# Performance work log

Measured on AMD Instinct MI355X. Metric: run time of the kernel, lower is better.

## Reference

```python
import jax, jax.numpy as jnp
import numpy as np

HID = 512
VOCAB = 1000


def _lstm_cell(x, h, c, w_ih, w_hh, b_ih, b_hh):
    # torch LSTMCell: gates order i, f, g, o
    gates = x @ w_ih.T + h @ w_hh.T + b_ih + b_hh
    i, f, g, o = jnp.split(gates, 4, axis=-1)
    i = jax.nn.sigmoid(i)
    f = jax.nn.sigmoid(f)
    g = jnp.tanh(g)
    o = jax.nn.sigmoid(o)
    c_new = f * c + i * g
    h_new = o * jnp.tanh(c_new)
    return h_new, c_new


def setup_inputs() -> dict:
    key = jax.random.key(0)
    ks = jax.random.split(key, 16)
    B, R, T = 64, 1024, 200
    s = 0.02
    return {
        "h": jax.random.normal(ks[0], (B, R, HID), dtype=jnp.float32),
        "y": jax.random.randint(ks[1], (B, T), 0, VOCAB, dtype=jnp.int32),
        "phi_w": jax.random.normal(ks[2], (HID, HID), jnp.float32) * s,
        "phi_b": jnp.zeros((HID,), jnp.float32),
        "psi_w": jax.random.normal(ks[3], (HID, HID), jnp.float32) * s,
        "psi_b": jnp.zeros((HID,), jnp.float32),
        "w_ih0": jax.random.normal(ks[4], (4 * HID, HID + VOCAB), jnp.float32) * s,
        "w_hh0": jax.random.normal(ks[5], (4 * HID, HID), jnp.float32) * s,
        "b_ih0": jnp.zeros((4 * HID,), jnp.float32),
        "b_hh0": jnp.zeros((4 * HID,), jnp.float32),
        "w_ih1": jax.random.normal(ks[6], (4 * HID, HID), jnp.float32) * s,
        "w_hh1": jax.random.normal(ks[7], (4 * HID, HID), jnp.float32) * s,
        "b_ih1": jnp.zeros((4 * HID,), jnp.float32),
        "b_hh1": jnp.zeros((4 * HID,), jnp.float32),
        "out_w": jax.random.normal(ks[8], (VOCAB, HID), jnp.float32) * s,
        "out_b": jnp.zeros((VOCAB,), jnp.float32),
    }


def reference(h, y, phi_w, phi_b, psi_w, psi_b,
              w_ih0, w_hh0, b_ih0, b_hh0,
              w_ih1, w_hh1, b_ih1, b_hh1,
              out_w, out_b):
    B = h.shape[0]
    # psi(h) is loop-invariant: precompute once. [B, R, HID]
    hp = h @ psi_w.T + psi_b
    # one-hot targets [T, B, VOCAB] (scan over time axis)
    y_oh = jax.nn.one_hot(y.T, VOCAB, dtype=h.dtype)

    zeros = jnp.zeros((B, HID), h.dtype)

    def step(carry, y_t):
        s0, cs0, s1, cs1 = carry
        # attention context on previous s1
        q = s1 @ phi_w.T + phi_b                  # [B, HID]
        e = jnp.einsum('bd,brd->br', q, hp)       # [B, R]
        alpha = jax.nn.softmax(e, axis=1)
        c = jnp.einsum('br,brd->bd', alpha, hp)   # [B, HID]
        inputs = jnp.concatenate([y_t, c], axis=1)
        s0, cs0 = _lstm_cell(inputs, s0, cs0, w_ih0, w_hh0, b_ih0, b_hh0)
        s1, cs1 = _lstm_cell(s0, s1, cs1, w_ih1, w_hh1, b_ih1, b_hh1)
        return (s0, cs0, s1, cs1), s1

    _, s_seq = jax.lax.scan(step, (zeros, zeros, zeros, zeros), y_oh)
    s_seq = jnp.transpose(s_seq, (1, 0, 2))       # [B, T, HID]
    return s_seq @ out_w.T + out_b                # [B, T, VOCAB]
```

## Files before the change

### kernel.cpp

```cpp
#include <hip/hip_runtime.h>
#include <math.h>

#define BB 64
#define RR 1024
#define TT 200
#define HH 512
#define VV 1000
#define GG 2048

__device__ __forceinline__ float sigmf(float x) { return 1.f / (1.f + __expf(-x)); }

__global__ __launch_bounds__(256) void transpose_k(const float* __restrict__ src,
    float* __restrict__ dst, int Msrc, int Mdst, int N, int sstride, int soff) {
  __shared__ float tile[32][33];
  int mt = blockIdx.y * 32, ntb = blockIdx.x * 32;
  int tx = threadIdx.x & 31, ty = threadIdx.x >> 5;
  #pragma unroll
  for (int i = ty; i < 32; i += 8) {
    int m = mt + i, n = ntb + tx;
    tile[i][tx] = (m < Msrc && n < N) ? src[(size_t)m * sstride + soff + n] : 0.f;
  }
  __syncthreads();
  #pragma unroll
  for (int i = ty; i < 32; i += 8) {
    int n = ntb + i, m = mt + tx;
    if (n < N && m < Mdst) dst[(size_t)n * Mdst + m] = tile[tx][i];
  }
}

__global__ __launch_bounds__(256) void biggemm_k(const float* __restrict__ A,
    const float* __restrict__ W, int wld, const float* __restrict__ bias,
    float* __restrict__ C, int cld, int Nout) {
  int mt = blockIdx.x * 128, nt = blockIdx.y * 64;
  __shared__ float As[16][132];
  __shared__ float Ws[16][68];
  int tid = threadIdx.x;
  int ty = tid >> 4, tx = tid & 15;
  float acc[8][4] = {};
  for (int k0 = 0; k0 < 512; k0 += 16) {
    {
      int kc = (tid & 3) * 4;
      int r0 = tid >> 2;
      #pragma unroll
      for (int hh = 0; hh < 2; hh++) {
        int row = r0 + hh * 64;
        float4 a4 = *(const float4*)&A[(size_t)(mt + row) * 512 + k0 + kc];
        As[kc + 0][row] = a4.x; As[kc + 1][row] = a4.y;
        As[kc + 2][row] = a4.z; As[kc + 3][row] = a4.w;
      }
      int krow = tid >> 4, nc = (tid & 15) * 4;
      *(float4*)&Ws[krow][nc] = *(const float4*)&W[(size_t)(k0 + krow) * wld + nt + nc];
    }
    __syncthreads();
    #pragma unroll
    for (int kk = 0; kk < 16; kk++) {
      float4 a0 = *(float4*)&As[kk][ty * 8];
      float4 a1 = *(float4*)&As[kk][ty * 8 + 4];
      float4 w4 = *(float4*)&Ws[kk][tx * 4];
      float av[8] = {a0.x, a0.y, a0.z, a0.w, a1.x, a1.y, a1.z, a1.w};
      float wv[4] = {w4.x, w4.y, w4.z, w4.w};
      #pragma unroll
      for (int i = 0; i < 8; i++)
        #pragma unroll
        for (int j = 0; j < 4; j++)
          acc[i][j] += av[i] * wv[j];
    }
    __syncthreads();
  }
  #pragma unroll
  for (int i = 0; i < 8; i++) {
    int m = mt + ty * 8 + i;
    #pragma unroll
    for (int j = 0; j < 4; j++) {
      int n = nt + tx * 4 + j;
      if (n < Nout) C[(size_t)m * cld + n] = acc[i][j] + bias[n];
    }
  }
}

__global__ __launch_bounds__(256) void smallgemm_k(
    const float* __restrict__ A1, const float* __restrict__ W1, int wld1,
    const float* __restrict__ A2, const float* __restrict__ W2, int wld2,
    int dual, float* __restrict__ Cpart, int N) {
  int nt = blockIdx.x, kc = blockIdx.y;
  const float *A, *W; int wld, k0;
  if (dual && kc >= 4) { A = A2; W = W2; wld = wld2; k0 = (kc - 4) * 128; }
  else                 { A = A1; W = W1; wld = wld1; k0 = kc * 128; }
  __shared__ float Ask[64][68];
  __shared__ float Ws[64][68];
  int tid = threadIdx.x;
  int bq = tid >> 4, nq = tid & 15;
  int b0 = bq * 4, n0 = nq * 4;
  float acc[4][4] = {};
  for (int kb = 0; kb < 128; kb += 64) {
    {
      int brow = tid & 63;
      int kcb = (tid >> 6) * 16;
      const float* ap = A + (size_t)brow * 512 + k0 + kb + kcb;
      #pragma unroll
      for (int j = 0; j < 4; j++) {
        float4 a4 = *(const float4*)(ap + j * 4);
        Ask[kcb + j * 4 + 0][brow] = a4.x;
        Ask[kcb + j * 4 + 1][brow] = a4.y;
        Ask[kcb + j * 4 + 2][brow] = a4.z;
        Ask[kcb + j * 4 + 3][brow] = a4.w;
      }
      int nc = (tid & 15) * 4;
      #pragma unroll
      for (int j = 0; j < 4; j++) {
        int krow = (tid >> 4) + j * 16;
        *(float4*)&Ws[krow][nc] =
            *(const float4*)&W[(size_t)(k0 + kb + krow) * wld + nt * 64 + nc];
      }
    }
    __syncthreads();
    #pragma unroll
    for (int kk = 0; kk < 64; kk++) {
      float4 a = *(float4*)&Ask[kk][b0];
      float4 w = *(float4*)&Ws[kk][n0];
      acc[0][0] += a.x * w.x; acc[0][1] += a.x * w.y; acc[0][2] += a.x * w.z; acc[0][3] += a.x * w.w;
      acc[1][0] += a.y * w.x; acc[1][1] += a.y * w.y; acc[1][2] += a.y * w.z; acc[1][3] += a.y * w.w;
      acc[2][0] += a.z * w.x; acc[2][1] += a.z * w.y; acc[2][2] += a.z * w.z; acc[2][3] += a.z * w.w;
      acc[3][0] += a.w * w.x; acc[3][1] += a.w * w.y; acc[3][2] += a.w * w.z; acc[3][3] += a.w * w.w;
    }
    __syncthreads();
  }
  float* Cout = Cpart + (size_t)kc * BB * N + (size_t)nt * 64;
  #pragma unroll
  for (int i = 0; i < 4; i++) {
    float4 v = make_float4(acc[i][0], acc[i][1], acc[i][2], acc[i][3]);
    *(float4*)&Cout[(size_t)(b0 + i) * N + n0] = v;
  }
}

__global__ __launch_bounds__(256) void attn_k(const float* __restrict__ hp,
    const float* __restrict__ qpart, const float* __restrict__ phi_b,
    float* __restrict__ partm, float* __restrict__ partl, float* __restrict__ partacc) {
  int b = blockIdx.x >> 3, ch = blockIdx.x & 7;
  __shared__ float qs[HH];
  __shared__ float wacc[4][HH];
  __shared__ float wml[8];
  int tid = threadIdx.x;
  for (int d = tid; d < HH; d += 256) {
    float v = phi_b[d];
    #pragma unroll
    for (int p = 0; p < 4; p++) v += qpart[((size_t)p * BB + b) * HH + d];
    qs[d] = v;
  }
  __syncthreads();
  int wave = tid >> 6, lane = tid & 63;
  float qreg[8];
  {
    const float* qp = qs + lane * 8;
    #pragma unroll
    for (int j = 0; j < 8; j++) qreg[j] = qp[j];
  }
  float m = -INFINITY, l = 0.f;
  float acc[8] = {0, 0, 0, 0, 0, 0, 0, 0};
  const float* hpb = hp + ((size_t)b * RR + ch * 128 + wave * 32) * HH + lane * 8;
  float4 v0 = *(const float4*)hpb;
  float4 v1 = *(const float4*)(hpb + 4);
  for (int i = 0; i < 32; i++) {
    float4 n0v, n1v;
    if (i < 31) {
      n0v = *(const float4*)(hpb + (size_t)(i + 1) * HH);
      n1v = *(const float4*)(hpb + (size_t)(i + 1) * HH + 4);
    }
    float rv[8] = {v0.x, v0.y, v0.z, v0.w, v1.x, v1.y, v1.z, v1.w};
    float d0 = 0.f;
    #pragma unroll
    for (int j = 0; j < 8; j++) d0 += qreg[j] * rv[j];
    #pragma unroll
    for (int off = 32; off > 0; off >>= 1) d0 += __shfl_xor(d0, off, 64);
    float mn = fmaxf(m, d0);
    float sc = __expf(m - mn);
    float w = __expf(d0 - mn);
    l = l * sc + w;
    #pragma unroll
    for (int j = 0; j < 8; j++) acc[j] = acc[j] * sc + w * rv[j];
    m = mn;
    v0 = n0v; v1 = n1v;
  }
  #pragma unroll
  for (int j = 0; j < 8; j++) wacc[wave][lane * 8 + j] = acc[j];
  if (lane == 0) { wml[wave] = m; wml[4 + wave] = l; }
  __syncthreads();
  float M = fmaxf(fmaxf(wml[0], wml[1]), fmaxf(wml[2], wml[3]));
  float e0 = __expf(wml[0] - M), e1 = __expf(wml[1] - M);
  float e2 = __expf(wml[2] - M), e3 = __expf(wml[3] - M);
  if (tid == 0) {
    partm[b * 8 + ch] = M;
    partl[b * 8 + ch] = wml[4] * e0 + wml[5] * e1 + wml[6] * e2 + wml[7] * e3;
  }
  for (int d = tid; d < HH; d += 256) {
    partacc[((size_t)b * 8 + ch) * HH + d] =
        wacc[0][d] * e0 + wacc[1][d] * e1 + wacc[2][d] * e2 + wacc[3][d] * e3;
  }
}

__global__ __launch_bounds__(256) void combine_k(const float* __restrict__ partm,
    const float* __restrict__ partl, const float* __restrict__ partacc,
    float* __restrict__ cbuf) {
  int b = blockIdx.x, tid = threadIdx.x;
  float M = -INFINITY;
  #pragma unroll
  for (int p = 0; p < 8; p++) M = fmaxf(M, partm[b * 8 + p]);
  float sc[8]; float L = 0.f;
  #pragma unroll
  for (int p = 0; p < 8; p++) { sc[p] = __expf(partm[b * 8 + p] - M); L += sc[p] * partl[b * 8 + p]; }
  float inv = 1.f / L;
  for (int d = tid; d < HH; d += 256) {
    float v = 0.f;
    #pragma unroll
    for (int p = 0; p < 8; p++) v += sc[p] * partacc[((size_t)b * 8 + p) * HH + d];
    cbuf[b * HH + d] = v * inv;
  }
}

__global__ __launch_bounds__(256) void act0_k(const float* __restrict__ gpart,
    const float* __restrict__ b_ih, const float* __restrict__ b_hh,
    const float* __restrict__ wyT, const int* __restrict__ y, int t,
    float* __restrict__ s0, float* __restrict__ cs0) {
  int idx = blockIdx.x * 256 + threadIdx.x;
  int b = idx >> 9, jj = idx & 511;
  int yv = y[b * TT + t];
  float g[4];
  #pragma unroll
  for (int gi = 0; gi < 4; gi++) {
    int j = gi * 512 + jj;
    float v = b_ih[j] + b_hh[j] + wyT[(size_t)yv * GG + j];
    #pragma unroll
    for (int p = 0; p < 8; p++) v += gpart[((size_t)p * BB + b) * GG + j];
    g[gi] = v;
  }
  float cn = sigmf(g[1]) * cs0[idx] + sigmf(g[0]) * tanhf(g[2]);
  cs0[idx] = cn;
  s0[idx] = sigmf(g[3]) * tanhf(cn);
}

__global__ __launch_bounds__(256) void act1_k(const float* __restrict__ gpart,
    const float* __restrict__ b_ih, const float* __restrict__ b_hh,
    int t, float* __restrict__ s1, float* __restrict__ cs1, float* __restrict__ s_seq) {
  int idx = blockIdx.x * 256 + threadIdx.x;
  int b = idx >> 9, jj = idx & 511;
  float g[4];
  #pragma unroll
  for (int gi = 0; gi < 4; gi++) {
    int j = gi * 512 + jj;
    float v = b_ih[j] + b_hh[j];
    #pragma unroll
    for (int p = 0; p < 8; p++) v += gpart[((size_t)p * BB + b) * GG + j];
    g[gi] = v;
  }
  float cn = sigmf(g[1]) * cs1[idx] + sigmf(g[0]) * tanhf(g[2]);
  cs1[idx] = cn;
  float h = sigmf(g[3]) * tanhf(cn);
  s1[idx] = h;
  s_seq[((size_t)b * TT + t) * HH + jj] = h;
}

extern "C" void kernel_launch(void* const* d_in, const int* in_sizes, int n_in,
                              void* d_out, int out_size, void* d_ws, size_t ws_size,
                              hipStream_t stream) {
  (void)in_sizes; (void)n_in; (void)out_size; (void)ws_size;
  const float* h     = (const float*)d_in[0];
  const int*   y     = (const int*)d_in[1];
  const float* phi_w = (const float*)d_in[2];
  const float* phi_b = (const float*)d_in[3];
  const float* psi_w = (const float*)d_in[4];
  const float* psi_b = (const float*)d_in[5];
  const float* w_ih0 = (const float*)d_in[6];
  const float* w_hh0 = (const float*)d_in[7];
  const float* b_ih0 = (const float*)d_in[8];
  const float* b_hh0 = (const float*)d_in[9];
  const float* w_ih1 = (const float*)d_in[10];
  const float* w_hh1 = (const float*)d_in[11];
  const float* b_ih1 = (const float*)d_in[12];
  const float* b_hh1 = (const float*)d_in[13];
  const float* out_w = (const float*)d_in[14];
  const float* out_b = (const float*)d_in[15];
  float* out = (float*)d_out;

  float* ws = (float*)d_ws;
  size_t off = 0;
  auto alloc = [&](size_t n) { size_t o = off; off += (n + 63) & ~(size_t)63; return o; };
  float* hp     = ws + alloc((size_t)BB * RR * HH);
  float* psi_wT = ws + alloc(HH * HH);
  float* phi_wT = ws + alloc(HH * HH);
  float* wc0T   = ws + alloc(HH * GG);
  float* whh0T  = ws + alloc(HH * GG);
  float* wih1T  = ws + alloc(HH * GG);
  float* whh1T  = ws + alloc(HH * GG);
  float* wyT    = ws + alloc((size_t)VV * GG);
  float* out_wT = ws + alloc((size_t)HH * 1024);
  float* st     = ws + alloc(4 * BB * HH);
  float* s0 = st, *cs0 = st + BB * HH, *s1 = st + 2 * BB * HH, *cs1 = st + 3 * BB * HH;
  float* qpart  = ws + alloc(4 * BB * HH);
  float* cbuf   = ws + alloc(BB * HH);
  float* g0part = ws + alloc((size_t)8 * BB * GG);
  float* g1part = ws + alloc((size_t)8 * BB * GG);
  float* partm  = ws + alloc(BB * 8);
  float* partl  = ws + alloc(BB * 8);
  float* partacc= ws + alloc((size_t)BB * 8 * HH);
  float* s_seq  = ws + alloc((size_t)BB * TT * HH);

  hipMemsetAsync(st, 0, (size_t)4 * BB * HH * sizeof(float), stream);

  dim3 tb(256);
  transpose_k<<<dim3(16, 16), tb, 0, stream>>>(psi_w, psi_wT, 512, 512, 512, 512, 0);
  transpose_k<<<dim3(16, 16), tb, 0, stream>>>(phi_w, phi_wT, 512, 512, 512, 512, 0);
  transpose_k<<<dim3(16, 64), tb, 0, stream>>>(w_ih0, wc0T, 2048, 2048, 512, 1512, 1000);
  transpose_k<<<dim3(16, 64), tb, 0, stream>>>(w_hh0, whh0T, 2048, 2048, 512, 512, 0);
  transpose_k<<<dim3(16, 64), tb, 0, stream>>>(w_ih1, wih1T, 2048, 2048, 512, 512, 0);
  transpose_k<<<dim3(16, 64), tb, 0, stream>>>(w_hh1, whh1T, 2048, 2048, 512, 512, 0);
  transpose_k<<<dim3(32, 64), tb, 0, stream>>>(w_ih0, wyT, 2048, 2048, 1000, 1512, 0);
  transpose_k<<<dim3(16, 32), tb, 0, stream>>>(out_w, out_wT, 1000, 1024, 512, 512, 0);

  biggemm_k<<<dim3(512, 8), tb, 0, stream>>>(h, psi_wT, 512, psi_b, hp, 512, 512);

  for (int t = 0; t < TT; t++) {
    smallgemm_k<<<dim3(8, 4), tb, 0, stream>>>(s1, phi_wT, 512, s1, phi_wT, 512, 0, qpart, 512);
    attn_k<<<dim3(512), tb, 0, stream>>>(hp, qpart, phi_b, partm, partl, partacc);
    combine_k<<<dim3(64), tb, 0, stream>>>(partm, partl, partacc, cbuf);
    smallgemm_k<<<dim3(32, 8), tb, 0, stream>>>(cbuf, wc0T, 2048, s0, whh0T, 2048, 1, g0part, 2048);
    act0_k<<<dim3(128), tb, 0, stream>>>(g0part, b_ih0, b_hh0, wyT, y, t, s0, cs0);
    smallgemm_k<<<dim3(32, 8), tb, 0, stream>>>(s0, wih1T, 2048, s1, whh1T, 2048, 1, g1part, 2048);
    act1_k<<<dim3(128), tb, 0, stream>>>(g1part, b_ih1, b_hh1, t, s1, cs1, s_seq);
  }

  biggemm_k<<<dim3(100, 16), tb, 0, stream>>>(s_seq, out_wT, 1024, out_b, out, 1000, 1000);
}
```

Before: 12.00 ms.

## Hoist recurrent-state GEMMs into one early launch and fuse attention combine into context GEMM

Each timestep's work is reorganized into fewer launches. A single early kernel computes the phi query projection and both hidden-to-hidden gate products (s0@Whh0, s1@Whh1), which depend only on the previous state. The attention softmax combine is fused into the context×Wc0 GEMM, removing the cbuf round trip. The remaining per-step GEMM handles only s0@Wih1. Separately, the big GEMM now uses a 128x128 tile with an 8x8 per-thread micro-tile, which raises register pressure.

After: 13.53 ms. 1.13x slower.

```diff
diff --git a/kernel.cpp b/kernel.cpp
--- a/kernel.cpp
+++ b/kernel.cpp
@@ -31,38 +31,36 @@
 __global__ __launch_bounds__(256) void biggemm_k(const float* __restrict__ A,
     const float* __restrict__ W, int wld, const float* __restrict__ bias,
     float* __restrict__ C, int cld, int Nout) {
-  int mt = blockIdx.x * 128, nt = blockIdx.y * 64;
+  int mt = blockIdx.x * 128, ntile = blockIdx.y * 128;
   __shared__ float As[16][132];
-  __shared__ float Ws[16][68];
+  __shared__ float Ws[16][132];
   int tid = threadIdx.x;
   int ty = tid >> 4, tx = tid & 15;
-  float acc[8][4] = {};
+  float acc[8][8] = {};
   for (int k0 = 0; k0 < 512; k0 += 16) {
     {
-      int kc = (tid & 3) * 4;
-      int r0 = tid >> 2;
-      #pragma unroll
-      for (int hh = 0; hh < 2; hh++) {
-        int row = r0 + hh * 64;
-        float4 a4 = *(const float4*)&A[(size_t)(mt + row) * 512 + k0 + kc];
-        As[kc + 0][row] = a4.x; As[kc + 1][row] = a4.y;
-        As[kc + 2][row] = a4.z; As[kc + 3][row] = a4.w;
-      }
-      int krow = tid >> 4, nc = (tid & 15) * 4;
-      *(float4*)&Ws[krow][nc] = *(const float4*)&W[(size_t)(k0 + krow) * wld + nt + nc];
+      int row = tid >> 1, kc = (tid & 1) * 8;
+      float4 a0 = *(const float4*)&A[(size_t)(mt + row) * 512 + k0 + kc];
+      float4 a1 = *(const float4*)&A[(size_t)(mt + row) * 512 + k0 + kc + 4];
+      As[kc + 0][row] = a0.x; As[kc + 1][row] = a0.y; As[kc + 2][row] = a0.z; As[kc + 3][row] = a0.w;
+      As[kc + 4][row] = a1.x; As[kc + 5][row] = a1.y; As[kc + 6][row] = a1.z; As[kc + 7][row] = a1.w;
+      int krow = tid >> 4, nc = (tid & 15) * 8;
+      *(float4*)&Ws[krow][nc]     = *(const float4*)&W[(size_t)(k0 + krow) * wld + ntile + nc];
+      *(float4*)&Ws[krow][nc + 4] = *(const float4*)&W[(size_t)(k0 + krow) * wld + ntile + nc + 4];
     }
     __syncthreads();
     #pragma unroll
     for (int kk = 0; kk < 16; kk++) {
       float4 a0 = *(float4*)&As[kk][ty * 8];
       float4 a1 = *(float4*)&As[kk][ty * 8 + 4];
-      float4 w4 = *(float4*)&Ws[kk][tx * 4];
+      float4 w0 = *(float4*)&Ws[kk][tx * 8];
+      float4 w1 = *(float4*)&Ws[kk][tx * 8 + 4];
       float av[8] = {a0.x, a0.y, a0.z, a0.w, a1.x, a1.y, a1.z, a1.w};
-      float wv[4] = {w4.x, w4.y, w4.z, w4.w};
+      float wv[8] = {w0.x, w0.y, w0.z, w0.w, w1.x, w1.y, w1.z, w1.w};
       #pragma unroll
       for (int i = 0; i < 8; i++)
         #pragma unroll
-        for (int j = 0; j < 4; j++)
+        for (int j = 0; j < 8; j++)
           acc[i][j] += av[i] * wv[j];
     }
     __syncthreads();
@@ -71,66 +69,96 @@
   for (int i = 0; i < 8; i++) {
     int m = mt + ty * 8 + i;
     #pragma unroll
-    for (int j = 0; j < 4; j++) {
-      int n = nt + tx * 4 + j;
+    for (int j = 0; j < 8; j++) {
+      int n = ntile + tx * 8 + j;
       if (n < Nout) C[(size_t)m * cld + n] = acc[i][j] + bias[n];
     }
   }
 }
 
-__global__ __launch_bounds__(256) void smallgemm_k(
-    const float* __restrict__ A1, const float* __restrict__ W1, int wld1,
-    const float* __restrict__ A2, const float* __restrict__ W2, int wld2,
-    int dual, float* __restrict__ Cpart, int N) {
+#define SG_BODY(Aptr, Wptr, wldv, k0v, Coutp, Nv, ntv)                                        \
+  {                                                                                           \
+    int tid = threadIdx.x;                                                                    \
+    int bq = tid >> 4, nq = tid & 15;                                                         \
+    int b0 = bq * 4, n0 = nq * 4;                                                             \
+    float acc[4][4] = {};                                                                     \
+    for (int kb = 0; kb < 128; kb += 64) {                                                    \
+      {                                                                                       \
+        int brow = tid & 63;                                                                  \
+        int kcb = (tid >> 6) * 16;                                                            \
+        const float* ap = (Aptr) + (size_t)brow * 512 + (k0v) + kb + kcb;                     \
+        _Pragma("unroll")                                                                     \
+        for (int j = 0; j < 4; j++) {                                                         \
+          float4 a4 = *(const float4*)(ap + j * 4);                                           \
+          Ask[kcb + j * 4 + 0][brow] = a4.x;                                                  \
+          Ask[kcb + j * 4 + 1][brow] = a4.y;                                                  \
+          Ask[kcb + j * 4 + 2][brow] = a4.z;                                                  \
+          Ask[kcb + j * 4 + 3][brow] = a4.w;                                                  \
+        }                                                                                     \
+        int nc = (tid & 15) * 4;                                                              \
+        _Pragma("unroll")                                                                     \
+        for (int j = 0; j < 4; j++) {                                                         \
+          int krow = (tid >> 4) + j * 16;                                                     \
+          *(float4*)&Wsk[krow][nc] =                                                          \
+              *(const float4*)&(Wptr)[(size_t)((k0v) + kb + krow) * (wldv) + (ntv)*64 + nc];  \
+        }                                                                                     \
+      }                                                                                       \
+      __syncthreads();                                                                        \
+      _Pragma("unroll")                                                                       \
+      for (int kk = 0; kk < 64; kk++) {                                                       \
+        float4 a = *(float4*)&Ask[kk][b0];                                                    \
+        float4 w = *(float4*)&Wsk[kk][n0];                                                    \
+        acc[0][0] += a.x * w.x; acc[0][1] += a.x * w.y; acc[0][2] += a.x * w.z; acc[0][3] += a.x * w.w; \
+        acc[1][0] += a.y * w.x; acc[1][1] += a.y * w.y; acc[1][2] += a.y * w.z; acc[1][3] += a.y * w.w; \
+        acc[2][0] += a.z * w.x; acc[2][1] += a.z * w.y; acc[2][2] += a.z * w.z; acc[2][3] += a.z * w.w; \
+        acc[3][0] += a.w * w.x; acc[3][1] += a.w * w.y; acc[3][2] += a.w * w.z; acc[3][3] += a.w * w.w; \
+      }                                                                                       \
+      __syncthreads();                                                                        \
+    }                                                                                         \
+    float* Cout2 = (Coutp) + (size_t)(ntv)*64;                                                \
+    _Pragma("unroll")                                                                         \
+    for (int i = 0; i < 4; i++) {                                                             \
+      float4 v = make_float4(acc[i][0], acc[i][1], acc[i][2], acc[i][3]);                     \
+      *(float4*)&Cout2[(size_t)(b0 + i) * (Nv) + n0] = v;                                     \
+    }                                                                                         \
+  }
+
+__global__ __launch_bounds__(256) void earlygemm_k(
+    const float* __restrict__ s0, const float* __restrict__ s1,
+    const float* __restrict__ phi_wT, const float* __restrict__ whh0T,
+    const float* __restrict__ whh1T,
+    float* __restrict__ qpart, float* __restrict__ g0part, float* __restrict__ g1part) {
+  __shared__ float Ask[64][68];
+  __shared__ float Wsk[64][68];
+  int bid = blockIdx.x;
+  const float *A, *W;
+  float* Cout;
+  int wld, k0, N, nt;
+  if (bid < 32) {
+    nt = bid & 7; int kc = bid >> 3;
+    A = s1; W = phi_wT; wld = 512; N = 512; k0 = kc * 128;
+    Cout = qpart + (size_t)kc * BB * 512;
+  } else if (bid < 160) {
+    int idx = bid - 32; nt = idx & 31; int kc = idx >> 5;
+    A = s0; W = whh0T; wld = GG; N = GG; k0 = kc * 128;
+    Cout = g0part + (size_t)(4 + kc) * BB * GG;
+  } else {
+    int idx = bid - 160; nt = idx & 31; int kc = idx >> 5;
+    A = s1; W = whh1T; wld = GG; N = GG; k0 = kc * 128;
+    Cout = g1part + (size_t)(4 + kc) * BB * GG;
+  }
+  SG_BODY(A, W, wld, k0, Cout, N, nt)
+}
+
+__global__ __launch_bounds__(256) void lategemm_k(
+    const float* __restrict__ s0, const float* __restrict__ wih1T,
+    float* __restrict__ g1part) {
+  __shared__ float Ask[64][68];
+  __shared__ float Wsk[64][68];
   int nt = blockIdx.x, kc = blockIdx.y;
-  const float *A, *W; int wld, k0;
-  if (dual && kc >= 4) { A = A2; W = W2; wld = wld2; k0 = (kc - 4) * 128; }
-  else                 { A = A1; W = W1; wld = wld1; k0 = kc * 128; }
-  __shared__ float Ask[64][68];
-  __shared__ float Ws[64][68];
-  int tid = threadIdx.x;
-  int bq = tid >> 4, nq = tid & 15;
-  int b0 = bq * 4, n0 = nq * 4;
-  float acc[4][4] = {};
-  for (int kb = 0; kb < 128; kb += 64) {
-    {
-      int brow = tid & 63;
-      int kcb = (tid >> 6) * 16;
-      const float* ap = A + (size_t)brow * 512 + k0 + kb + kcb;
-      #pragma unroll
-      for (int j = 0; j < 4; j++) {
-        float4 a4 = *(const float4*)(ap + j * 4);
-        Ask[kcb + j * 4 + 0][brow] = a4.x;
-        Ask[kcb + j * 4 + 1][brow] = a4.y;
-        Ask[kcb + j * 4 + 2][brow] = a4.z;
-        Ask[kcb + j * 4 + 3][brow] = a4.w;
-      }
-      int nc = (tid & 15) * 4;
-      #pragma unroll
-      for (int j = 0; j < 4; j++) {
-        int krow = (tid >> 4) + j * 16;
-        *(float4*)&Ws[krow][nc] =
-            *(const float4*)&W[(size_t)(k0 + kb + krow) * wld + nt * 64 + nc];
-      }
-    }
-    __syncthreads();
-    #pragma unroll
-    for (int kk = 0; kk < 64; kk++) {
-      float4 a = *(float4*)&Ask[kk][b0];
-      float4 w = *(float4*)&Ws[kk][n0];
-      acc[0][0] += a.x * w.x; acc[0][1] += a.x * w.y; acc[0][2] += a.x * w.z; acc[0][3] += a.x * w.w;
-      acc[1][0] += a.y * w.x; acc[1][1] += a.y * w.y; acc[1][2] += a.y * w.z; acc[1][3] += a.y * w.w;
-      acc[2][0] += a.z * w.x; acc[2][1] += a.z * w.y; acc[2][2] += a.z * w.z; acc[2][3] += a.z * w.w;
-      acc[3][0] += a.w * w.x; acc[3][1] += a.w * w.y; acc[3][2] += a.w * w.z; acc[3][3] += a.w * w.w;
-    }
-    __syncthreads();
-  }
-  float* Cout = Cpart + (size_t)kc * BB * N + (size_t)nt * 64;
-  #pragma unroll
-  for (int i = 0; i < 4; i++) {
-    float4 v = make_float4(acc[i][0], acc[i][1], acc[i][2], acc[i][3]);
-    *(float4*)&Cout[(size_t)(b0 + i) * N + n0] = v;
-  }
+  int k0 = kc * 128;
+  float* Cout = g1part + (size_t)kc * BB * GG;
+  SG_BODY(s0, wih1T, GG, k0, Cout, GG, nt)
 }
 
 __global__ __launch_bounds__(256) void attn_k(const float* __restrict__ hp,
@@ -198,22 +226,79 @@
   }
 }
 
-__global__ __launch_bounds__(256) void combine_k(const float* __restrict__ partm,
-    const float* __restrict__ partl, const float* __restrict__ partacc,
-    float* __restrict__ cbuf) {
-  int b = blockIdx.x, tid = threadIdx.x;
-  float M = -INFINITY;
-  #pragma unroll
-  for (int p = 0; p < 8; p++) M = fmaxf(M, partm[b * 8 + p]);
-  float sc[8]; float L = 0.f;
-  #pragma unroll
-  for (int p = 0; p < 8; p++) { sc[p] = __expf(partm[b * 8 + p] - M); L += sc[p] * partl[b * 8 + p]; }
-  float inv = 1.f / L;
-  for (int d = tid; d < HH; d += 256) {
-    float v = 0.f;
-    #pragma unroll
-    for (int p = 0; p < 8; p++) v += sc[p] * partacc[((size_t)b * 8 + p) * HH + d];
-    cbuf[b * HH + d] = v * inv;
+__global__ __launch_bounds__(256) void gemmc_k(
+    const float* __restrict__ partm, const float* __restrict__ partl,
+    const float* __restrict__ partacc, const float* __restrict__ wc0T,
+    float* __restrict__ g0part) {
+  int nt = blockIdx.x, kc = blockIdx.y;
+  __shared__ float csl[128][66];
+  __shared__ float Wsk[64][68];
+  __shared__ float scs[64][8];
+  __shared__ float sinv[64];
+  int tid = threadIdx.x;
+  if (tid < 64) {
+    int b = tid;
+    float M = -INFINITY;
+    #pragma unroll
+    for (int p = 0; p < 8; p++) M = fmaxf(M, partm[b * 8 + p]);
+    float L = 0.f;
+    #pragma unroll
+    for (int p = 0; p < 8; p++) {
+      float s = __expf(partm[b * 8 + p] - M);
+      scs[b][p] = s;
+      L += s * partl[b * 8 + p];
+    }
+    sinv[b] = 1.f / L;
+  }
+  __syncthreads();
+  {
+    int b = tid >> 2, jq = tid & 3;
+    float inv = sinv[b];
+    #pragma unroll
+    for (int j4 = 0; j4 < 8; j4++) {
+      int j = jq * 32 + j4 * 4;
+      float ax = 0.f, ay = 0.f, az = 0.f, aw = 0.f;
+      #pragma unroll
+      for (int p = 0; p < 8; p++) {
+        float s = scs[b][p];
+        float4 v = *(const float4*)&partacc[((size_t)b * 8 + p) * HH + kc * 128 + j];
+        ax += s * v.x; ay += s * v.y; az += s * v.z; aw += s * v.w;
+      }
+      csl[j + 0][b] = ax * inv; csl[j + 1][b] = ay * inv;
+      csl[j + 2][b] = az * inv; csl[j + 3][b] = aw * inv;
+    }
+  }
+  __syncthreads();
+  int bq = tid >> 4, nq = tid & 15;
+  int b0 = bq * 4, n0 = nq * 4;
+  float acc[4][4] = {};
+  for (int kb = 0; kb < 128; kb += 64) {
+    {
+      int nc = (tid & 15) * 4;
+      #pragma unroll
+      for (int j = 0; j < 4; j++) {
+        int krow = (tid >> 4) + j * 16;
+        *(float4*)&Wsk[krow][nc] =
+            *(const float4*)&wc0T[(size_t)(kc * 128 + kb + krow) * GG + nt * 64 + nc];
+      }
+    }
+    __syncthreads();
+    #pragma unroll
+    for (int kk = 0; kk < 64; kk++) {
+      float4 a = *(float4*)&csl[kb + kk][b0];
+      float4 w = *(float4*)&Wsk[kk][n0];
+      acc[0][0] += a.x * w.x; acc[0][1] += a.x * w.y; acc[0][2] += a.x * w.z; acc[0][3] += a.x * w.w;
+      acc[1][0] += a.y * w.x; acc[1][1] += a.y * w.y; acc[1][2] += a.y * w.z; acc[1][3] += a.y * w.w;
+      acc[2][0] += a.z * w.x; acc[2][1] += a.z * w.y; acc[2][2] += a.z * w.z; acc[2][3] += a.z * w.w;
+      acc[3][0] += a.w * w.x; acc[3][1] += a.w * w.y; acc[3][2] += a.w * w.z; acc[3][3] += a.w * w.w;
+    }
+    __syncthreads();
+  }
+  float* Cout = g0part + (size_t)kc * BB * GG + (size_t)nt * 64;
+  #pragma unroll
+  for (int i = 0; i < 4; i++) {
+    float4 v = make_float4(acc[i][0], acc[i][1], acc[i][2], acc[i][3]);
+    *(float4*)&Cout[(size_t)(b0 + i) * GG + n0] = v;
   }
 }
 
@@ -296,7 +381,6 @@
   float* st     = ws + alloc(4 * BB * HH);
   float* s0 = st, *cs0 = st + BB * HH, *s1 = st + 2 * BB * HH, *cs1 = st + 3 * BB * HH;
   float* qpart  = ws + alloc(4 * BB * HH);
-  float* cbuf   = ws + alloc(BB * HH);
   float* g0part = ws + alloc((size_t)8 * BB * GG);
   float* g1part = ws + alloc((size_t)8 * BB * GG);
   float* partm  = ws + alloc(BB * 8);
@@ -316,17 +400,17 @@
   transpose_k<<<dim3(32, 64), tb, 0, stream>>>(w_ih0, wyT, 2048, 2048, 1000, 1512, 0);
   transpose_k<<<dim3(16, 32), tb, 0, stream>>>(out_w, out_wT, 1000, 1024, 512, 512, 0);
 
-  biggemm_k<<<dim3(512, 8), tb, 0, stream>>>(h, psi_wT, 512, psi_b, hp, 512, 512);
+  biggemm_k<<<dim3(512, 4), tb, 0, stream>>>(h, psi_wT, 512, psi_b, hp, 512, 512);
 
   for (int t = 0; t < TT; t++) {
-    smallgemm_k<<<dim3(8, 4), tb, 0, stream>>>(s1, phi_wT, 512, s1, phi_wT, 512, 0, qpart, 512);
+    earlygemm_k<<<dim3(288), tb, 0, stream>>>(s0, s1, phi_wT, whh0T, whh1T,
+                                              qpart, g0part, g1part);
     attn_k<<<dim3(512), tb, 0, stream>>>(hp, qpart, phi_b, partm, partl, partacc);
-    combine_k<<<dim3(64), tb, 0, stream>>>(partm, partl, partacc, cbuf);
-    smallgemm_k<<<dim3(32, 8), tb, 0, stream>>>(cbuf, wc0T, 2048, s0, whh0T, 2048, 1, g0part, 2048);
+    gemmc_k<<<dim3(32, 4), tb, 0, stream>>>(partm, partl, partacc, wc0T, g0part);
     act0_k<<<dim3(128), tb, 0, stream>>>(g0part, b_ih0, b_hh0, wyT, y, t, s0, cs0);
-    smallgemm_k<<<dim3(32, 8), tb, 0, stream>>>(s0, wih1T, 2048, s1, whh1T, 2048, 1, g1part, 2048);
+    lategemm_k<<<dim3(32, 4), tb, 0, stream>>>(s0, wih1T, g1part);
     act1_k<<<dim3(128), tb, 0, stream>>>(g1part, b_ih1, b_hh1, t, s1, cs1, s_seq);
   }
 
-  biggemm_k<<<dim3(100, 16), tb, 0, stream>>>(s_seq, out_wT, 1024, out_b, out, 1000, 1000);
-}
+  biggemm_k<<<dim3(100, 8), tb, 0, stream>>>(s_seq, out_wT, 1024, out_b, out, 1000, 1000);
+}
```
